# Performance work log

Hardware: AMD Instinct MI355X
Metric: run time of the kernel (lower is better)

## Reference

```python
import jax, jax.numpy as jnp
import numpy as np

DT = 1.0
SEQ, BATCH, HID = 2048, 512, 256

def setup_inputs() -> dict:
    key = jax.random.key(0)
    ks = jax.random.split(key, 4)
    x = jax.random.normal(ks[0], (SEQ, BATCH, 1), dtype=jnp.float32)
    # small init scale keeps tanh unsaturated and the Euler recurrence stable
    W1 = 0.3 * jax.random.normal(ks[1], (2, HID), dtype=jnp.float32)
    b1 = jnp.zeros((HID,), jnp.float32)
    W2 = (0.3 / np.sqrt(HID)) * jax.random.normal(ks[2], (HID, HID), dtype=jnp.float32)
    b2 = jnp.zeros((HID,), jnp.float32)
    W3 = (0.1 / np.sqrt(HID)) * jax.random.normal(ks[3], (HID, 1), dtype=jnp.float32)
    b3 = jnp.zeros((1,), jnp.float32)
    state0 = jnp.zeros((BATCH,), jnp.float32)
    return {"x": x, "W1": W1, "b1": b1, "W2": W2, "b2": b2, "W3": W3, "b3": b3, "state0": state0}

def reference(x, W1, b1, W2, b2, W3, b3, state0):
    # Forward-Euler ODE integration: y[n+1] = y[n] + dt * f(x[n], y[n]).
    # Torch code returns odeint_output[:-1, :, None], i.e. the state at each
    # step BEFORE the update, with shape identical to x.
    xs = x[:, :, 0]  # (seq, batch) -- derivative_network.input = x.squeeze(2)

    def f(x_t, y):
        u = jnp.stack([x_t, y], axis=-1)          # (B, 2)
        h = jnp.tanh(u @ W1 + b1)                 # (B, H)
        h = jnp.tanh(h @ W2 + b2)                 # (B, H)
        return (h @ W3 + b3)[:, 0]                # (B,)

    def step(state, x_t):
        new_state = state + DT * f(x_t, state)
        return new_state, state                   # emit pre-update state

    _, ys = jax.lax.scan(step, state0, xs)        # ys: (seq, batch)
    return ys[:, :, None]                         # (seq, batch, 1), same shape as x
```

## Files before the change

kernel.cpp:

```cpp
#include <hip/hip_runtime.h>


#define SEQ 2048
#define BATCH 512
#define HID 256

typedef __bf16 bf16x8 __attribute__((ext_vector_type(8)));
typedef short short8 __attribute__((ext_vector_type(8)));
typedef float f32x4 __attribute__((ext_vector_type(4)));

__device__ __forceinline__ unsigned short f2bf_rne(float f) {
  unsigned u = __builtin_bit_cast(unsigned, f);
  u += 0x7fffu + ((u >> 16) & 1u);
  return (unsigned short)(u >> 16);
}

__device__ __forceinline__ float tanh_pade(float x) {
  float cx = __builtin_amdgcn_fmed3f(x, -4.5f, 4.5f);
  float u = cx * cx;
  float num = cx * (10395.f + u * (1260.f + 21.f * u));
  float den = 10395.f + u * (4725.f + u * (210.f + u));
  return num * __builtin_amdgcn_rcpf(den);
}

__device__ __forceinline__ float row16_sum_to_lane15(float v) {
  int s;
  s = __builtin_amdgcn_update_dpp(0, __builtin_bit_cast(int, v), 0x111, 0xf, 0xf, true);
  v += __builtin_bit_cast(float, s);
  s = __builtin_amdgcn_update_dpp(0, __builtin_bit_cast(int, v), 0x112, 0xf, 0xf, true);
  v += __builtin_bit_cast(float, s);
  s = __builtin_amdgcn_update_dpp(0, __builtin_bit_cast(int, v), 0x114, 0xf, 0xf, true);
  v += __builtin_bit_cast(float, s);
  s = __builtin_amdgcn_update_dpp(0, __builtin_bit_cast(int, v), 0x118, 0xf, 0xf, true);
  v += __builtin_bit_cast(float, s);
  return v;
}

__global__ void pack_w2_kernel(const float* __restrict__ W2,
                               unsigned short* __restrict__ ws) {
  int idx = blockIdx.x * 256 + threadIdx.x;
  int e    = idx & 7;
  int l    = (idx >> 3) & 63;
  int kc   = (idx >> 9) & 7;
  int tile = idx >> 12;
  int k = kc * 32 + (l >> 4) * 8 + e;
  int c = tile * 16 + (l & 15);
  ws[idx] = f2bf_rne(W2[k * HID + c]);
}

__global__ __launch_bounds__(512, 2) void odenet_kernel(
    const float* __restrict__ x, const float* __restrict__ W1,
    const float* __restrict__ b1, const unsigned short* __restrict__ wsW2,
    const float* __restrict__ b2, const float* __restrict__ W3,
    const float* __restrict__ b3, const float* __restrict__ state0,
    float* __restrict__ out) {
  __shared__ __align__(16) unsigned short A_lds[2 * HID];
  __shared__ __align__(16) float partial[2][8];

  const int tid  = threadIdx.x;
  const int lane = tid & 63;
  const int wave = tid >> 6;
  const int rh   = tid >> 8;
  const int j    = tid & 255;
  const int b0   = blockIdx.x * 2;

  const float w10 = W1[j];
  const float w11 = W1[HID + j];
  const float b1j = b1[j];
  const float b3v = b3[0];
  const int   c0   = wave * 32 + (lane & 15);
  const int   c1   = c0 + 16;
  const float b2c0 = b2[c0], b2c1 = b2[c1];
  const float w3c0 = W3[c0], w3c1 = W3[c1];

  short8 bf0[8], bf1[8];
  {
    const short8* wp = (const short8*)wsW2;
    const int t0 = wave * 2, t1 = t0 + 1;
#pragma unroll
    for (int kc = 0; kc < 8; ++kc) {
      bf0[kc] = wp[(t0 * 8 + kc) * 64 + lane];
      bf1[kc] = wp[(t1 * 8 + kc) * 64 + lane];
    }
  }

  const short8 zero8 = {0, 0, 0, 0, 0, 0, 0, 0};
  short8 areg[8];
#pragma unroll
  for (int kc = 0; kc < 8; ++kc) areg[kc] = zero8;
  const bool aread = ((lane & 15) < 2);
  const int  aoff  = (lane & 15) * HID + (lane >> 4) * 8;

  float y = state0[b0 + rh];

  const float* xp = x + b0 + rh;
  float* yo = out + b0 + rh;

  float xb[8], xn[8], xa[8];
#pragma unroll
  for (int i = 0; i < 8; ++i) xb[i] = xp[i * BATCH];
#pragma unroll
  for (int i = 0; i < 8; ++i) xa[i] = xb[i] * w10 + b1j;

  for (int tb = 0; tb < SEQ; tb += 8) {
    if (tb + 8 < SEQ) {
      const float* xq = xp + (tb + 8) * BATCH;
#pragma unroll
      for (int i = 0; i < 8; ++i) xn[i] = xq[i * BATCH];
    }

#pragma unroll
    for (int i = 0; i < 8; ++i) {
      const int t = tb + i;

      const float pre = __builtin_fmaf(y, w11, xa[i]);
      A_lds[tid & 511] = f2bf_rne(tanh_pade(pre));
      __syncthreads();

      if (aread) {
#pragma unroll
        for (int kc = 0; kc < 8; ++kc)
          areg[kc] = *(const short8*)&A_lds[aoff + kc * 32];
      }

      f32x4 a00 = {0.f, 0.f, 0.f, 0.f};
      f32x4 a10 = {0.f, 0.f, 0.f, 0.f};
      f32x4 a01 = {0.f, 0.f, 0.f, 0.f};
      f32x4 a11 = {0.f, 0.f, 0.f, 0.f};
#pragma unroll
      for (int kc = 0; kc < 4; ++kc) {
        const bf16x8 aL = __builtin_bit_cast(bf16x8, areg[kc]);
        const bf16x8 aH = __builtin_bit_cast(bf16x8, areg[kc + 4]);
        a00 = __builtin_amdgcn_mfma_f32_16x16x32_bf16(
            aL, __builtin_bit_cast(bf16x8, bf0[kc]), a00, 0, 0, 0);
        a10 = __builtin_amdgcn_mfma_f32_16x16x32_bf16(
            aL, __builtin_bit_cast(bf16x8, bf1[kc]), a10, 0, 0, 0);
        a01 = __builtin_amdgcn_mfma_f32_16x16x32_bf16(
            aH, __builtin_bit_cast(bf16x8, bf0[kc + 4]), a01, 0, 0, 0);
        a11 = __builtin_amdgcn_mfma_f32_16x16x32_bf16(
            aH, __builtin_bit_cast(bf16x8, bf1[kc + 4]), a11, 0, 0, 0);
      }
      const f32x4 acc0 = a00 + a01;
      const f32x4 acc1 = a10 + a11;

      float p0 = 0.f, p1 = 0.f;
      if (lane < 16) {
        p0 = tanh_pade(acc0[0] + b2c0) * w3c0 + tanh_pade(acc1[0] + b2c1) * w3c1;
        p1 = tanh_pade(acc0[1] + b2c0) * w3c0 + tanh_pade(acc1[1] + b2c1) * w3c1;
      }
      p0 = row16_sum_to_lane15(p0);
      p1 = row16_sum_to_lane15(p1);
      if (lane == 15) {
        partial[0][wave] = p0;
        partial[1][wave] = p1;
      }
      __syncthreads();

      const f32x4 q0 = *(const f32x4*)&partial[rh][0];
      const f32x4 q1 = *(const f32x4*)&partial[rh][4];
      const float f = ((q0[0] + q0[1]) + (q0[2] + q0[3])) +
                      ((q1[0] + q1[1]) + (q1[2] + q1[3])) + b3v;
      const float y_old = y;
      y += f;
      if (j == 0) yo[t * BATCH] = y_old;
    }

    if (tb + 8 < SEQ) {
#pragma unroll
      for (int i = 0; i < 8; ++i) xb[i] = xn[i];
#pragma unroll
      for (int i = 0; i < 8; ++i) xa[i] = xb[i] * w10 + b1j;
    }
  }
}

extern "C" void kernel_launch(void* const* d_in, const int* in_sizes, int n_in,
                              void* d_out, int out_size, void* d_ws, size_t ws_size,
                              hipStream_t stream) {
  const float* x  = (const float*)d_in[0];
  const float* W1 = (const float*)d_in[1];
  const float* b1 = (const float*)d_in[2];
  const float* W2 = (const float*)d_in[3];
  const float* b2 = (const float*)d_in[4];
  const float* W3 = (const float*)d_in[5];
  const float* b3 = (const float*)d_in[6];
  const float* s0 = (const float*)d_in[7];
  unsigned short* ws = (unsigned short*)d_ws;
  float* out = (float*)d_out;

  pack_w2_kernel<<<256, 256, 0, stream>>>(W2, ws);
  odenet_kernel<<<256, 512, 0, stream>>>(x, W1, b1, ws, b2, W3, b3, s0, out);
}
```

Before: 1.463 ms.

## Use 4 waves per block, each computing 64 output columns with W2 in registers

Cuts the block from 8 waves to 4, so each wave holds four 16-column W2 tiles in registers and issues 32 MFMAs per step instead of 16. Each thread now computes the first-layer activations for both batch rows. Fewer waves should make the two per-step barriers cheaper and shrink the cross-wave reduction to four partials. The cost is a longer serial MFMA chain per wave and more registers per thread on the latency-bound recurrence.

Measured after the change: 1.445 ms. No clear change (-1.2%).

```diff
diff --git a/kernel.cpp b/kernel.cpp
--- a/kernel.cpp
+++ b/kernel.cpp
@@ -48,73 +48,82 @@
   ws[idx] = f2bf_rne(W2[k * HID + c]);
 }
 
-__global__ __launch_bounds__(512, 2) void odenet_kernel(
+__global__ __launch_bounds__(256, 1) void odenet_kernel(
     const float* __restrict__ x, const float* __restrict__ W1,
     const float* __restrict__ b1, const unsigned short* __restrict__ wsW2,
     const float* __restrict__ b2, const float* __restrict__ W3,
     const float* __restrict__ b3, const float* __restrict__ state0,
     float* __restrict__ out) {
   __shared__ __align__(16) unsigned short A_lds[2 * HID];
-  __shared__ __align__(16) float partial[2][8];
+  __shared__ __align__(16) float partial[2][4];
 
   const int tid  = threadIdx.x;
   const int lane = tid & 63;
   const int wave = tid >> 6;
-  const int rh   = tid >> 8;
-  const int j    = tid & 255;
+  const int j    = tid;
   const int b0   = blockIdx.x * 2;
 
   const float w10 = W1[j];
   const float w11 = W1[HID + j];
   const float b1j = b1[j];
   const float b3v = b3[0];
-  const int   c0   = wave * 32 + (lane & 15);
-  const int   c1   = c0 + 16;
-  const float b2c0 = b2[c0], b2c1 = b2[c1];
-  const float w3c0 = W3[c0], w3c1 = W3[c1];
+  float b2c[4], w3c[4];
+#pragma unroll
+  for (int t = 0; t < 4; ++t) {
+    const int c = wave * 64 + t * 16 + (lane & 15);
+    b2c[t] = b2[c];
+    w3c[t] = W3[c];
+  }
 
-  short8 bf0[8], bf1[8];
+  short8 bf[4][8];
   {
     const short8* wp = (const short8*)wsW2;
-    const int t0 = wave * 2, t1 = t0 + 1;
 #pragma unroll
-    for (int kc = 0; kc < 8; ++kc) {
-      bf0[kc] = wp[(t0 * 8 + kc) * 64 + lane];
-      bf1[kc] = wp[(t1 * 8 + kc) * 64 + lane];
-    }
+    for (int t = 0; t < 4; ++t)
+#pragma unroll
+      for (int kc = 0; kc < 8; ++kc)
+        bf[t][kc] = wp[((wave * 4 + t) * 8 + kc) * 64 + lane];
   }
 
   const short8 zero8 = {0, 0, 0, 0, 0, 0, 0, 0};
   short8 areg[8];
 #pragma unroll
   for (int kc = 0; kc < 8; ++kc) areg[kc] = zero8;
-  const bool aread = ((lane & 15) < 2);
-  const int  aoff  = (lane & 15) * HID + (lane >> 4) * 8;
+  const bool aread = ((lane & 11) == 0);
+  const int  arow  = (lane >> 2) & 1;
+  const int  aoff  = arow * HID + (lane >> 4) * 8;
 
-  float y = state0[b0 + rh];
+  float y0 = state0[b0];
+  float y1 = state0[b0 + 1];
 
-  const float* xp = x + b0 + rh;
-  float* yo = out + b0 + rh;
+  const float* xp = x + b0;
+  float* yo = out + b0;
 
-  float xb[8], xn[8], xa[8];
+  float2 xb[8], xn[8];
+  float xa0[8], xa1[8];
 #pragma unroll
-  for (int i = 0; i < 8; ++i) xb[i] = xp[i * BATCH];
+  for (int i = 0; i < 8; ++i) xb[i] = *(const float2*)&xp[i * BATCH];
 #pragma unroll
-  for (int i = 0; i < 8; ++i) xa[i] = xb[i] * w10 + b1j;
+  for (int i = 0; i < 8; ++i) {
+    xa0[i] = xb[i].x * w10 + b1j;
+    xa1[i] = xb[i].y * w10 + b1j;
+  }
 
   for (int tb = 0; tb < SEQ; tb += 8) {
     if (tb + 8 < SEQ) {
       const float* xq = xp + (tb + 8) * BATCH;
 #pragma unroll
-      for (int i = 0; i < 8; ++i) xn[i] = xq[i * BATCH];
+      for (int i = 0; i < 8; ++i) xn[i] = *(const float2*)&xq[i * BATCH];
     }
 
 #pragma unroll
     for (int i = 0; i < 8; ++i) {
       const int t = tb + i;
 
-      const float pre = __builtin_fmaf(y, w11, xa[i]);
-      A_lds[tid & 511] = f2bf_rne(tanh_pade(pre));
+      const float pre0 = __builtin_fmaf(y0, w11, xa0[i]);
+      const float pre1 = __builtin_fmaf(y1, w11, xa1[i]);
+      A_lds[j]       = f2bf_rne(tanh_pade(pre0));
+      A_lds[HID + j] = f2bf_rne(tanh_pade(pre1));
       __syncthreads();
 
       if (aread) {
@@ -123,53 +132,50 @@
           areg[kc] = *(const short8*)&A_lds[aoff + kc * 32];
       }
 
-      f32x4 a00 = {0.f, 0.f, 0.f, 0.f};
-      f32x4 a10 = {0.f, 0.f, 0.f, 0.f};
-      f32x4 a01 = {0.f, 0.f, 0.f, 0.f};
-      f32x4 a11 = {0.f, 0.f, 0.f, 0.f};
+      f32x4 acc[4];
 #pragma unroll
-      for (int kc = 0; kc < 4; ++kc) {
-        const bf16x8 aL = __builtin_bit_cast(bf16x8, areg[kc]);
-        const bf16x8 aH = __builtin_bit_cast(bf16x8, areg[kc + 4]);
-        a00 = __builtin_amdgcn_mfma_f32_16x16x32_bf16(
-            aL, __builtin_bit_cast(bf16x8, bf0[kc]), a00, 0, 0, 0);
-        a10 = __builtin_amdgcn_mfma_f32_16x16x32_bf16(
-            aL, __builtin_bit_cast(bf16x8, bf1[kc]), a10, 0, 0, 0);
-        a01 = __builtin_amdgcn_mfma_f32_16x16x32_bf16(
-            aH, __builtin_bit_cast(bf16x8, bf0[kc + 4]), a01, 0, 0, 0);
-        a11 = __builtin_amdgcn_mfma_f32_16x16x32_bf16(
-            aH, __builtin_bit_cast(bf16x8, bf1[kc + 4]), a11, 0, 0, 0);
+      for (int t4 = 0; t4 < 4; ++t4) acc[t4] = f32x4{0.f, 0.f, 0.f, 0.f};
+#pragma unroll
+      for (int kc = 0; kc < 8; ++kc) {
+        const bf16x8 a = __builtin_bit_cast(bf16x8, areg[kc]);
+#pragma unroll
+        for (int t4 = 0; t4 < 4; ++t4)
+          acc[t4] = __builtin_amdgcn_mfma_f32_16x16x32_bf16(
+              a, __builtin_bit_cast(bf16x8, bf[t4][kc]), acc[t4], 0, 0, 0);
       }
-      const f32x4 acc0 = a00 + a01;
-      const f32x4 acc1 = a10 + a11;
 
-      float p0 = 0.f, p1 = 0.f;
-      if (lane < 16) {
-        p0 = tanh_pade(acc0[0] + b2c0) * w3c0 + tanh_pade(acc1[0] + b2c1) * w3c1;
-        p1 = tanh_pade(acc0[1] + b2c0) * w3c0 + tanh_pade(acc1[1] + b2c1) * w3c1;
+      float s = 0.f;
+      if (lane < 32) {
+#pragma unroll
+        for (int t4 = 0; t4 < 4; ++t4)
+          s += tanh_pade(acc[t4][0] + b2c[t4]) * w3c[t4];
       }
-      p0 = row16_sum_to_lane15(p0);
-      p1 = row16_sum_to_lane15(p1);
-      if (lane == 15) {
-        partial[0][wave] = p0;
-        partial[1][wave] = p1;
-      }
+      s = row16_sum_to_lane15(s);
+      if ((lane & 15) == 15 && lane < 32)
+        partial[lane >> 4][wave] = s;
       __syncthreads();
 
-      const f32x4 q0 = *(const f32x4*)&partial[rh][0];
-      const f32x4 q1 = *(const f32x4*)&partial[rh][4];
-      const float f = ((q0[0] + q0[1]) + (q0[2] + q0[3])) +
-                      ((q1[0] + q1[1]) + (q1[2] + q1[3])) + b3v;
-      const float y_old = y;
-      y += f;
-      if (j == 0) yo[t * BATCH] = y_old;
+      const f32x4 q0 = *(const f32x4*)&partial[0][0];
+      const f32x4 q1 = *(const f32x4*)&partial[1][0];
+      const float f0 = ((q0[0] + q0[1]) + (q0[2] + q0[3])) + b3v;
+      const float f1 = ((q1[0] + q1[1]) + (q1[2] + q1[3])) + b3v;
+      const float y0o = y0, y1o = y1;
+      y0 += f0;
+      y1 += f1;
+      if (tid == 0) {
+        float2 o{y0o, y1o};
+        *(float2*)&yo[t * BATCH] = o;
+      }
     }
 
     if (tb + 8 < SEQ) {
 #pragma unroll
       for (int i = 0; i < 8; ++i) xb[i] = xn[i];
 #pragma unroll
-      for (int i = 0; i < 8; ++i) xa[i] = xb[i] * w10 + b1j;
+      for (int i = 0; i < 8; ++i) {
+        xa0[i] = xb[i].x * w10 + b1j;
+        xa1[i] = xb[i].y * w10 + b1j;
+      }
     }
   }
 }
@@ -189,5 +195,5 @@
   float* out = (float*)d_out;
 
   pack_w2_kernel<<<256, 256, 0, stream>>>(W2, ws);
-  odenet_kernel<<<256, 512, 0, stream>>>(x, W1, b1, ws, b2, W3, b3, s0, out);
+  odenet_kernel<<<256, 256, 0, stream>>>(x, W1, b1, ws, b2, W3, b3, s0, out);
 }
```
